# Performance work log

Measured on AMD Instinct MI355X. Metric: run time of the kernel, lower is better.

The kernel has to match this reference:

```python
import jax, jax.numpy as jnp
import numpy as np

D_MODEL = 1024
N_HEADS = 16
HEAD_DIM = D_MODEL // N_HEADS


def setup_inputs() -> dict:
    key = jax.random.key(0)
    k1, k2, k3 = jax.random.split(key, 3)
    B, T, C = 4, 2048, D_MODEL
    x = jax.random.normal(k1, (B, T, C), dtype=jnp.float32)
    # torch Linear weight is (out,in); store as (in,out) so y = x @ W
    w_qkv = jax.random.normal(k2, (C, 3 * C), dtype=jnp.float32) * (1.0 / np.sqrt(C))
    w_proj = jax.random.normal(k3, (C, C), dtype=jnp.float32) * (1.0 / np.sqrt(C))
    return {"x": x, "w_qkv": w_qkv, "w_proj": w_proj}


def reference(x, w_qkv, w_proj):
    B, T, C = x.shape
    H, Dh = N_HEADS, HEAD_DIM
    qkv = x @ w_qkv                        # (B,T,3C)
    q, k, v = jnp.split(qkv, 3, axis=-1)
    def heads(t):
        return t.reshape(B, T, H, Dh).transpose(0, 2, 1, 3)  # (B,H,T,Dh)
    q, k, v = heads(q), heads(k), heads(v)
    scores = jnp.einsum('bhqd,bhkd->bhqk', q, k) / np.sqrt(Dh).astype(np.float32)
    causal = jnp.tril(jnp.ones((T, T), dtype=bool))
    scores = jnp.where(causal, scores, -jnp.inf)
    attn = jax.nn.softmax(scores, axis=-1)
    y = jnp.einsum('bhqk,bhkd->bhqd', attn, v)  # (B,H,T,Dh)
    y = y.transpose(0, 2, 1, 3).reshape(B, T, C)
    return y @ w_proj
```

## Files before the change

kernel.cpp:

```cpp
#include <hip/hip_runtime.h>

#define SEQ_T 2048
#define NBATCH 4
#define CDIM 1024
#define NHEAD 16
#define MROWS 8192
#define QKVC 3072

typedef unsigned short u16;
typedef __bf16 bf16x8 __attribute__((ext_vector_type(8)));
typedef float f32x4 __attribute__((ext_vector_type(4)));
typedef float f32x16 __attribute__((ext_vector_type(16)));
typedef unsigned short u16x8 __attribute__((ext_vector_type(8)));
typedef unsigned uint32x4 __attribute__((ext_vector_type(4)));

__device__ __forceinline__ u16 f32_to_bf16(float f) {
  union { float f; unsigned int u; } v; v.f = f;
  unsigned int u = v.u;
  unsigned int r = ((u >> 16) & 1u) + 0x7fffu;
  return (u16)((u + r) >> 16);
}

__device__ __forceinline__ void gload_lds16(const u16* g, u16* l) {
  __builtin_amdgcn_global_load_lds(
      (const __attribute__((address_space(1))) void*)g,
      (__attribute__((address_space(3))) void*)l, 16, 0, 0);
}


__global__ __launch_bounds__(256) void cast_block_kernel(const float* __restrict__ in,
                                                         u16* __restrict__ out) {
  const int i = blockIdx.x * 256 + threadIdx.x;
  const int kg = i & 127;
  const int row = i >> 7;
  const float4 v0 = ((const float4*)in)[i * 2];
  const float4 v1 = ((const float4*)in)[i * 2 + 1];
  union { u16 u[8]; bf16x8 b; } o;
  o.u[0] = f32_to_bf16(v0.x); o.u[1] = f32_to_bf16(v0.y);
  o.u[2] = f32_to_bf16(v0.z); o.u[3] = f32_to_bf16(v0.w);
  o.u[4] = f32_to_bf16(v1.x); o.u[5] = f32_to_bf16(v1.y);
  o.u[6] = f32_to_bf16(v1.z); o.u[7] = f32_to_bf16(v1.w);
  const int tile = (row >> 4) * 32 + (kg >> 2);
  const int lane = (row & 15) + ((kg & 3) << 4);
  *(bf16x8*)(out + (size_t)tile * 512 + lane * 8) = o.b;
}

__global__ void transpose_cast_block_kernel(const float* __restrict__ in,
                                            u16* __restrict__ out, int Cc) {
  __shared__ float tile[32][33];
  const int c0 = blockIdx.x * 32, r0 = blockIdx.y * 32;
  const int tx = threadIdx.x, ty = threadIdx.y;
  #pragma unroll
  for (int i = 0; i < 32; i += 8)
    tile[ty + i][tx] = in[(size_t)(r0 + ty + i) * Cc + c0 + tx];
  __syncthreads();
  const int t = ty * 32 + tx;
  if (t < 128) {
    const int cc = t & 31, kgq = t >> 5;
    union { u16 u[8]; bf16x8 b; } o;
    #pragma unroll
    for (int j = 0; j < 8; ++j) o.u[j] = f32_to_bf16(tile[kgq * 8 + j][cc]);
    const int rowN = c0 + cc;
    const int tileI = (rowN >> 4) * 32 + (r0 >> 5);
    const int lane = (rowN & 15) + (kgq << 4);
    *(bf16x8*)(out + (size_t)tileI * 512 + lane * 8) = o.b;
  }
}

__global__ __launch_bounds__(256, 3)
void gemm1_kernel(const u16* __restrict__ Ab, const u16* __restrict__ Bb,
                  u16* __restrict__ Qb, u16* __restrict__ Kc, u16* __restrict__ Vc) {
  __shared__ u16 lds[24576];
  const int tid = threadIdx.x;
  const int lane = tid & 63, w = tid >> 6;
  const int wm = w >> 1, wn = w & 1;
  const int l15 = lane & 15, lhi = lane >> 4;
  const int row0 = blockIdx.x * 128, col0 = blockIdx.y * 128;
  const int rt0 = row0 >> 4, ct0 = col0 >> 4;

  const u16* aT = Ab + (size_t)(rt0 + w * 2) * 16384 + lane * 8;
  const u16* bT = Bb + (size_t)(ct0 + w * 2) * 16384 + lane * 8;

  f32x4 acc[4][4] = {};

#define SA(S) (lds + (S) * 4096)
#define SB(S) (lds + 12288 + (S) * 4096)
#define STAGE(KT, S)                                                            \
  {                                                                             \
    gload_lds16(aT + (size_t)(KT) * 512,         SA(S) + (w * 2) * 512);        \
    gload_lds16(aT + 16384 + (size_t)(KT) * 512, SA(S) + (w * 2 + 1) * 512);    \
    gload_lds16(bT + (size_t)(KT) * 512,         SB(S) + (w * 2) * 512);        \
    gload_lds16(bT + 16384 + (size_t)(KT) * 512, SB(S) + (w * 2 + 1) * 512);    \
  }
#define COMPUTE(S)                                                              \
  {                                                                             \
    bf16x8 af[4], bf[4];                                                        \
    _Pragma("unroll") for (int mi = 0; mi < 4; ++mi)                            \
      af[mi] = *(const bf16x8*)(SA(S) + (wm * 4 + mi) * 512 + lane * 8);        \
    _Pragma("unroll") for (int ni = 0; ni < 4; ++ni)                            \
      bf[ni] = *(const bf16x8*)(SB(S) + (wn * 4 + ni) * 512 + lane * 8);        \
    __builtin_amdgcn_s_setprio(1);                                              \
    _Pragma("unroll") for (int mi = 0; mi < 4; ++mi)                            \
      _Pragma("unroll") for (int ni = 0; ni < 4; ++ni)                          \
        acc[mi][ni] = __builtin_amdgcn_mfma_f32_16x16x32_bf16(af[mi], bf[ni],   \
                                                              acc[mi][ni], 0, 0, 0); \
    __builtin_amdgcn_s_setprio(0);                                              \
  }
#define WAITBAR4                                                                \
  asm volatile("s_waitcnt vmcnt(4)" ::: "memory");                              \
  __builtin_amdgcn_sched_barrier(0);                                            \
  __builtin_amdgcn_s_barrier();

  STAGE(0, 0);
  STAGE(1, 1);
  WAITBAR4;

  #pragma unroll 1
  for (int kt = 0; kt < 30; kt += 3) {
    STAGE(kt + 2, 2); COMPUTE(0); WAITBAR4;
    STAGE(kt + 3, 0); COMPUTE(1); WAITBAR4;
    STAGE(kt + 4, 1); COMPUTE(2); WAITBAR4;
  }
  COMPUTE(0);
  asm volatile("s_waitcnt vmcnt(0)" ::: "memory");
  __builtin_amdgcn_sched_barrier(0);
  __builtin_amdgcn_s_barrier();
  COMPUTE(1);
#undef STAGE
#undef COMPUTE
#undef WAITBAR4
#undef SA
#undef SB

  const int region = col0 >> 10;
  if (region == 0) {
    #pragma unroll
    for (int mt = 0; mt < 4; ++mt)
      #pragma unroll
      for (int nt = 0; nt < 4; ++nt)
        #pragma unroll
        for (int r = 0; r < 4; ++r) {
          const int rr = row0 + wm * 64 + mt * 16 + lhi * 4 + r;
          const int cc = col0 + wn * 64 + nt * 16 + l15;
          Qb[(size_t)rr * CDIM + cc] = f32_to_bf16(acc[mt][nt][r] * 0.18033688011f);
        }
  } else {
    __syncthreads();
    if (region == 1) {
      #pragma unroll
      for (int mt = 0; mt < 4; ++mt)
        #pragma unroll
        for (int nt = 0; nt < 4; ++nt)
          #pragma unroll
          for (int r = 0; r < 4; ++r) {
            const int sidx = wn * 8192 + (wm * 2 + (mt >> 1)) * 2048
                           + nt * 512
                           + ((mt & 1) * 16 + lhi * 4 + r + ((l15 >> 3) & 1) * 32) * 8
                           + (l15 & 7);
            lds[sidx] = f32_to_bf16(acc[mt][nt][r]);
          }
    } else {
      #pragma unroll
      for (int mt = 0; mt < 4; ++mt)
        #pragma unroll
        for (int nt = 0; nt < 4; ++nt)
          #pragma unroll
          for (int r = 0; r < 4; ++r) {
            const int sidx = wn * 8192 + (wm * 2 + (mt >> 1)) * 2048
                           + ((mt & 1) * 2 + (nt >> 1)) * 512
                           + ((nt & 1) * 16 + l15 + 32 * (lhi >> 1)) * 8
                           + (lhi & 1) * 4 + r;
            lds[sidx] = f32_to_bf16(acc[mt][nt][r]);
          }
    }
    __syncthreads();
    u16* dstB = (region == 1) ? Kc : Vc;
    const int bb = row0 >> 11;
    const int kv0b = (row0 & 2047) >> 5;
    const int hbase = (col0 & 1023) >> 6;
    #pragma unroll
    for (int hh = 0; hh < 2; ++hh) {
      u16* dst = dstB + (size_t)(bb * 16 + hbase + hh) * 131072 + (size_t)kv0b * 2048;
      const u16* src = lds + hh * 8192;
      #pragma unroll
      for (int c = 0; c < 4; ++c) {
        const int o = (c * 256 + tid) * 8;
        *(uint32x4*)(dst + o) = *(const uint32x4*)(src + o);
      }
    }
  }
}

__global__ __launch_bounds__(256, 3)
void gemm2_kernel(const u16* __restrict__ Ab, const u16* __restrict__ Bb,
                  float* __restrict__ C) {
  __shared__ u16 lds[24576];
  const int tid = threadIdx.x;
  const int lane = tid & 63, w = tid >> 6;
  const int wm = w >> 1, wn = w & 1;
  const int l15 = lane & 15, lhi = lane >> 4;
  const int row0 = blockIdx.x * 128, col0 = blockIdx.y * 128;
  const int rt0 = row0 >> 4, ct0 = col0 >> 4;

  const u16* aT = Ab + (size_t)(rt0 + w * 2) * 16384 + lane * 8;
  const u16* bT = Bb + (size_t)(ct0 + w * 2) * 16384 + lane * 8;

  f32x4 acc[4][4] = {};

#define SA(S) (lds + (S) * 4096)
#define SB(S) (lds + 12288 + (S) * 4096)
#define STAGE(KT, S)                                                            \
  {                                                                             \
    gload_lds16(aT + (size_t)(KT) * 512,         SA(S) + (w * 2) * 512);        \
    gload_lds16(aT + 16384 + (size_t)(KT) * 512, SA(S) + (w * 2 + 1) * 512);    \
    gload_lds16(bT + (size_t)(KT) * 512,         SB(S) + (w * 2) * 512);        \
    gload_lds16(bT + 16384 + (size_t)(KT) * 512, SB(S) + (w * 2 + 1) * 512);    \
  }
#define COMPUTE(S)                                                              \
  {                                                                             \
    bf16x8 af[4], bf[4];                                                        \
    _Pragma("unroll") for (int mi = 0; mi < 4; ++mi)                            \
      af[mi] = *(const bf16x8*)(SA(S) + (wm * 4 + mi) * 512 + lane * 8);        \
    _Pragma("unroll") for (int ni = 0; ni < 4; ++ni)                            \
      bf[ni] = *(const bf16x8*)(SB(S) + (wn * 4 + ni) * 512 + lane * 8);        \
    __builtin_amdgcn_s_setprio(1);                                              \
    _Pragma("unroll") for (int mi = 0; mi < 4; ++mi)                            \
      _Pragma("unroll") for (int ni = 0; ni < 4; ++ni)                          \
        acc[mi][ni] = __builtin_amdgcn_mfma_f32_16x16x32_bf16(af[mi], bf[ni],   \
                                                              acc[mi][ni], 0, 0, 0); \
    __builtin_amdgcn_s_setprio(0);                                              \
  }
#define WAITBAR4                                                                \
  asm volatile("s_waitcnt vmcnt(4)" ::: "memory");                              \
  __builtin_amdgcn_sched_barrier(0);                                            \
  __builtin_amdgcn_s_barrier();

  STAGE(0, 0);
  STAGE(1, 1);
  WAITBAR4;

  #pragma unroll 1
  for (int kt = 0; kt < 30; kt += 3) {
    STAGE(kt + 2, 2); COMPUTE(0); WAITBAR4;
    STAGE(kt + 3, 0); COMPUTE(1); WAITBAR4;
    STAGE(kt + 4, 1); COMPUTE(2); WAITBAR4;
  }
  COMPUTE(0);
  asm volatile("s_waitcnt vmcnt(0)" ::: "memory");
  __builtin_amdgcn_sched_barrier(0);
  __builtin_amdgcn_s_barrier();
  COMPUTE(1);
#undef STAGE
#undef COMPUTE
#undef WAITBAR4
#undef SA
#undef SB

  #pragma unroll
  for (int mt = 0; mt < 4; ++mt)
    #pragma unroll
    for (int nt = 0; nt < 4; ++nt)
      #pragma unroll
      for (int r = 0; r < 4; ++r) {
        const int rr = row0 + wm * 64 + mt * 16 + lhi * 4 + r;
        const int cc = col0 + wn * 64 + nt * 16 + l15;
        C[(size_t)rr * CDIM + cc] = acc[mt][nt][r];
      }
}

template <bool DOMASK>
__device__ __forceinline__ void attn_step32(const bf16x8 (&qf)[4],
                                            const bf16x8 (&kf)[4],
                                            const bf16x8 (&vb)[2][2],
                                            const bf16x8 ones,
                                            f32x16 (&acc)[2], f32x16& acc1,
                                            int l31, int lhi5, int kv0, int qg) {
  f32x16 st = {};
  #pragma unroll
  for (int i = 0; i < 4; ++i)
    st = __builtin_amdgcn_mfma_f32_32x32x16_bf16(kf[i], qf[i], st, 0, 0, 0);
  #pragma unroll
  for (int g = 0; g < 16; ++g) {
    float sv = st[g];
    if (DOMASK) {
      const int kvg = kv0 + (g & 3) + 8 * (g >> 2) + 4 * lhi5;
      sv = (kvg > qg) ? -__builtin_inff() : sv;
    }
    st[g] = exp2f(sv);
  }
  unsigned c0, c1, c2, c3, c4, c5, c6, c7;
  asm("v_cvt_pk_bf16_f32 %0, %1, %2" : "=v"(c0) : "v"(st[0]),  "v"(st[1]));
  asm("v_cvt_pk_bf16_f32 %0, %1, %2" : "=v"(c1) : "v"(st[2]),  "v"(st[3]));
  asm("v_cvt_pk_bf16_f32 %0, %1, %2" : "=v"(c2) : "v"(st[4]),  "v"(st[5]));
  asm("v_cvt_pk_bf16_f32 %0, %1, %2" : "=v"(c3) : "v"(st[6]),  "v"(st[7]));
  asm("v_cvt_pk_bf16_f32 %0, %1, %2" : "=v"(c4) : "v"(st[8]),  "v"(st[9]));
  asm("v_cvt_pk_bf16_f32 %0, %1, %2" : "=v"(c5) : "v"(st[10]), "v"(st[11]));
  asm("v_cvt_pk_bf16_f32 %0, %1, %2" : "=v"(c6) : "v"(st[12]), "v"(st[13]));
  asm("v_cvt_pk_bf16_f32 %0, %1, %2" : "=v"(c7) : "v"(st[14]), "v"(st[15]));
  asm("v_permlane32_swap_b32 %0, %1" : "+v"(c0), "+v"(c2));
  asm("v_permlane32_swap_b32 %0, %1" : "+v"(c1), "+v"(c3));
  asm("v_permlane32_swap_b32 %0, %1" : "+v"(c4), "+v"(c6));
  asm("v_permlane32_swap_b32 %0, %1" : "+v"(c5), "+v"(c7));
  uint32x4 p0w, p1w;
  p0w[0] = c0; p0w[1] = c1; p0w[2] = c2; p0w[3] = c3;
  p1w[0] = c4; p1w[1] = c5; p1w[2] = c6; p1w[3] = c7;
  const bf16x8 pa0 = __builtin_bit_cast(bf16x8, p0w);
  const bf16x8 pa1 = __builtin_bit_cast(bf16x8, p1w);
  acc[0] = __builtin_amdgcn_mfma_f32_32x32x16_bf16(pa0, vb[0][0], acc[0], 0, 0, 0);
  acc[0] = __builtin_amdgcn_mfma_f32_32x32x16_bf16(pa1, vb[1][0], acc[0], 0, 0, 0);
  acc[1] = __builtin_amdgcn_mfma_f32_32x32x16_bf16(pa0, vb[0][1], acc[1], 0, 0, 0);
  acc[1] = __builtin_amdgcn_mfma_f32_32x32x16_bf16(pa1, vb[1][1], acc[1], 0, 0, 0);
  acc1 = __builtin_amdgcn_mfma_f32_32x32x16_bf16(pa0, ones, acc1, 0, 0, 0);
  acc1 = __builtin_amdgcn_mfma_f32_32x32x16_bf16(pa1, ones, acc1, 0, 0, 0);
}

__global__ __launch_bounds__(256, 2) void attn_kernel(const u16* __restrict__ Qb,
                                                      const u16* __restrict__ Kc,
                                                      const u16* __restrict__ Vc,
                                                      u16* __restrict__ Yb) {
  __shared__ u16 Kl[2][4096];
  __shared__ u16 Vl[2][4096];
  const int tid = threadIdx.x, lane = tid & 63, wid = tid >> 6;
  const int l31 = lane & 31, lhi5 = lane >> 5;
  const int id = blockIdx.x;
  const int xcd = id & 7, graw = (id >> 3) & 7, hi3 = id >> 6;
  const int g = (hi3 & 4) ? (7 - graw) : graw;
  const int bh = hi3 * 8 + xcd;
  const int b = bh >> 4, h = bh & 15;
  const int pa = g * 4 + wid;
  const int qA0 = pa * 32, qB0 = (63 - pa) * 32;
  const int nchA = pa + 1, nchB = 64 - pa;
  const int nc2max = 32 - 2 * g;
  const u16* Qp  = Qb + (size_t)b * SEQ_T * CDIM + h * 64;
  const u16* KcC = Kc + (size_t)bh * 131072;
  const u16* VcC = Vc + (size_t)bh * 131072;

  u16x8 ou;
  #pragma unroll
  for (int j = 0; j < 8; ++j) ou[j] = 0x3F80;
  const bf16x8 ones = __builtin_bit_cast(bf16x8, ou);

  gload_lds16(KcC + wid * 512 + lane * 8,        &Kl[0][wid * 512]);
  gload_lds16(KcC + 2048 + wid * 512 + lane * 8, &Kl[0][2048 + wid * 512]);
  gload_lds16(VcC + wid * 512 + lane * 8,        &Vl[0][wid * 512]);
  gload_lds16(VcC + 2048 + wid * 512 + lane * 8, &Vl[0][2048 + wid * 512]);

  bf16x8 qfA[4], qfB[4];
  #pragma unroll
  for (int i = 0; i < 4; ++i) {
    qfA[i] = *(const bf16x8*)(Qp + (size_t)(qA0 + l31) * CDIM + i * 16 + lhi5 * 8);
    qfB[i] = *(const bf16x8*)(Qp + (size_t)(qB0 + l31) * CDIM + i * 16 + lhi5 * 8);
  }
  const int qgA = qA0 + l31, qgB = qB0 + l31;

  f32x16 accA[2] = {}, accB[2] = {};
  f32x16 acc1A = {}, acc1B = {};

  __syncthreads();

  int cbuf = 0;
  for (int ic2 = 0; ic2 < nc2max; ++ic2) {
    if (ic2 + 1 < nc2max) {
      const u16* kg = KcC + (size_t)(ic2 + 1) * 4096 + wid * 512 + lane * 8;
      const u16* vg = VcC + (size_t)(ic2 + 1) * 4096 + wid * 512 + lane * 8;
      gload_lds16(kg,        &Kl[cbuf ^ 1][wid * 512]);
      gload_lds16(kg + 2048, &Kl[cbuf ^ 1][2048 + wid * 512]);
      gload_lds16(vg,        &Vl[cbuf ^ 1][wid * 512]);
      gload_lds16(vg + 2048, &Vl[cbuf ^ 1][2048 + wid * 512]);
    }
    #pragma unroll
    for (int h2 = 0; h2 < 2; ++h2) {
      const int c = ic2 * 2 + h2;
      const u16* kb = &Kl[cbuf][h2 * 2048];
      const u16* vp = &Vl[cbuf][h2 * 2048];
      bf16x8 kf[4], vb[2][2];
      #pragma unroll
      for (int i = 0; i < 4; ++i)
        kf[i] = *(const bf16x8*)(kb + i * 512 + lane * 8);
      #pragma unroll
      for (int kk = 0; kk < 2; ++kk)
        #pragma unroll
        for (int dh = 0; dh < 2; ++dh)
          vb[kk][dh] = *(const bf16x8*)(vp + (kk * 2 + dh) * 512 + lane * 8);

      const int kv0 = c * 32;
      if (c < nchB) {
        if (c == nchB - 1)
          attn_step32<true>(qfB, kf, vb, ones, accB, acc1B, l31, lhi5, kv0, qgB);
        else
          attn_step32<false>(qfB, kf, vb, ones, accB, acc1B, l31, lhi5, kv0, qgB);
      }
      if (c < nchA) {
        if (c == nchA - 1)
          attn_step32<true>(qfA, kf, vb, ones, accA, acc1A, l31, lhi5, kv0, qgA);
        else
          attn_step32<false>(qfA, kf, vb, ones, accA, acc1A, l31, lhi5, kv0, qgA);
      }
    }
    __syncthreads();
    cbuf ^= 1;
  }

  #pragma unroll
  for (int g2 = 0; g2 < 16; ++g2) {
    const int qlA = (g2 & 3) + 8 * (g2 >> 2) + 4 * lhi5;
    const float ivA = 1.0f / acc1A[g2];
    const float ivB = 1.0f / acc1B[g2];
    const int laneb = ((qlA & 15)) + ((l31 >> 3) << 4);
    const int jj = l31 & 7;
    #pragma unroll
    for (int dh = 0; dh < 2; ++dh) {
      const int qA = qA0 + qlA;
      const int qB = qB0 + qlA;
      const size_t rrA = (size_t)b * 2048 + qA;
      const size_t rrB = (size_t)b * 2048 + qB;
      Yb[((rrA >> 4) * 32 + h * 2 + dh) * 512 + laneb * 8 + jj] =
          f32_to_bf16(accA[dh][g2] * ivA);
      Yb[((rrB >> 4) * 32 + h * 2 + dh) * 512 + laneb * 8 + jj] =
          f32_to_bf16(accB[dh][g2] * ivB);
    }
  }
}

extern "C" void kernel_launch(void* const* d_in, const int* in_sizes, int n_in,
                              void* d_out, int out_size, void* d_ws, size_t ws_size,
                              hipStream_t stream) {
  const float* x      = (const float*)d_in[0];
  const float* w_qkv  = (const float*)d_in[1];
  const float* w_proj = (const float*)d_in[2];
  float* out = (float*)d_out;

  u16* Xb  = (u16*)d_ws;
  u16* Wqt = Xb  + (size_t)MROWS * CDIM;
  u16* Wpt = Wqt + (size_t)QKVC * CDIM;
  u16* Qb  = Wpt + (size_t)CDIM * CDIM;
  u16* Kc  = Qb  + (size_t)MROWS * CDIM;
  u16* Vc  = Kc  + (size_t)64 * 131072;
  u16* Yb  = Vc  + (size_t)64 * 131072;

  cast_block_kernel<<<MROWS * CDIM / 8 / 256, 256, 0, stream>>>(x, Xb);
  transpose_cast_block_kernel<<<dim3(QKVC / 32, CDIM / 32), dim3(32, 8), 0, stream>>>(w_qkv, Wqt, QKVC);
  transpose_cast_block_kernel<<<dim3(CDIM / 32, CDIM / 32), dim3(32, 8), 0, stream>>>(w_proj, Wpt, CDIM);

  gemm1_kernel<<<dim3(MROWS / 128, QKVC / 128), 256, 0, stream>>>(Xb, Wqt, Qb, Kc, Vc);

  attn_kernel<<<512, 256, 0, stream>>>(Qb, Kc, Vc, Yb);

  gemm2_kernel<<<dim3(MROWS / 128, CDIM / 128), 256, 0, stream>>>(Yb, Wpt, out);
}
```

Baseline: 158.9 us.

## Give each attention wave one query tile and double the grid

The attention kernel now assigns each wave a single 32-row query tile, where before each wave handled a pair of causally balanced tiles. Blocks combine two low and two high tiles so total work stays balanced, and the grid doubles to 1024 blocks with launch bounds raised to 4 blocks per CU. This cuts register pressure to raise occupancy and spreads work over more blocks. In exchange, K/V tiles are loaded into LDS twice as often in total, the K/V fragments read from LDS are shared by one query tile instead of two, and waves in a block finish at different times and idle at the barriers.

```diff
diff --git a/kernel.cpp b/kernel.cpp
--- a/kernel.cpp
+++ b/kernel.cpp
@@ -314,7 +314,7 @@
   acc1 = __builtin_amdgcn_mfma_f32_32x32x16_bf16(pa1, ones, acc1, 0, 0, 0);
 }
 
-__global__ __launch_bounds__(256, 2) void attn_kernel(const u16* __restrict__ Qb,
+__global__ __launch_bounds__(256, 4) void attn_kernel(const u16* __restrict__ Qb,
                                                       const u16* __restrict__ Kc,
                                                       const u16* __restrict__ Vc,
                                                       u16* __restrict__ Yb) {
@@ -323,14 +323,14 @@
   const int tid = threadIdx.x, lane = tid & 63, wid = tid >> 6;
   const int l31 = lane & 31, lhi5 = lane >> 5;
   const int id = blockIdx.x;
-  const int xcd = id & 7, graw = (id >> 3) & 7, hi3 = id >> 6;
-  const int g = (hi3 & 4) ? (7 - graw) : graw;
+  const int xcd = id & 7, g = (id >> 3) & 15, hi3 = id >> 7;
   const int bh = hi3 * 8 + xcd;
   const int b = bh >> 4, h = bh & 15;
-  const int pa = g * 4 + wid;
-  const int qA0 = pa * 32, qB0 = (63 - pa) * 32;
-  const int nchA = pa + 1, nchB = 64 - pa;
-  const int nc2max = 32 - 2 * g;
+  const int jw = (wid == 0) ? 2 * g : (wid == 1) ? 2 * g + 1
+               : (wid == 2) ? 63 - 2 * g : 62 - 2 * g;
+  const int q0 = jw * 32;
+  const int nch = jw + 1;
+  const int nc2max = 32 - g;
   const u16* Qp  = Qb + (size_t)b * SEQ_T * CDIM + h * 64;
   const u16* KcC = Kc + (size_t)bh * 131072;
   const u16* VcC = Vc + (size_t)bh * 131072;
@@ -345,16 +345,14 @@
   gload_lds16(VcC + wid * 512 + lane * 8,        &Vl[0][wid * 512]);
   gload_lds16(VcC + 2048 + wid * 512 + lane * 8, &Vl[0][2048 + wid * 512]);
 
-  bf16x8 qfA[4], qfB[4];
-  #pragma unroll
-  for (int i = 0; i < 4; ++i) {
-    qfA[i] = *(const bf16x8*)(Qp + (size_t)(qA0 + l31) * CDIM + i * 16 + lhi5 * 8);
-    qfB[i] = *(const bf16x8*)(Qp + (size_t)(qB0 + l31) * CDIM + i * 16 + lhi5 * 8);
-  }
-  const int qgA = qA0 + l31, qgB = qB0 + l31;
-
-  f32x16 accA[2] = {}, accB[2] = {};
-  f32x16 acc1A = {}, acc1B = {};
+  bf16x8 qf[4];
+  #pragma unroll
+  for (int i = 0; i < 4; ++i)
+    qf[i] = *(const bf16x8*)(Qp + (size_t)(q0 + l31) * CDIM + i * 16 + lhi5 * 8);
+  const int qg = q0 + l31;
+
+  f32x16 acc[2] = {};
+  f32x16 acc1 = {};
 
   __syncthreads();
 
@@ -371,30 +369,24 @@
     #pragma unroll
     for (int h2 = 0; h2 < 2; ++h2) {
       const int c = ic2 * 2 + h2;
-      const u16* kb = &Kl[cbuf][h2 * 2048];
-      const u16* vp = &Vl[cbuf][h2 * 2048];
-      bf16x8 kf[4], vb[2][2];
-      #pragma unroll
-      for (int i = 0; i < 4; ++i)
-        kf[i] = *(const bf16x8*)(kb + i * 512 + lane * 8);
-      #pragma unroll
-      for (int kk = 0; kk < 2; ++kk)
+      if (c < nch) {
+        const u16* kb = &Kl[cbuf][h2 * 2048];
+        const u16* vp = &Vl[cbuf][h2 * 2048];
+        bf16x8 kf[4], vb[2][2];
         #pragma unroll
-        for (int dh = 0; dh < 2; ++dh)
-          vb[kk][dh] = *(const bf16x8*)(vp + (kk * 2 + dh) * 512 + lane * 8);
-
-      const int kv0 = c * 32;
-      if (c < nchB) {
-        if (c == nchB - 1)
-          attn_step32<true>(qfB, kf, vb, ones, accB, acc1B, l31, lhi5, kv0, qgB);
+        for (int i = 0; i < 4; ++i)
+          kf[i] = *(const bf16x8*)(kb + i * 512 + lane * 8);
+        #pragma unroll
+        for (int kk = 0; kk < 2; ++kk)
+          #pragma unroll
+          for (int dh = 0; dh < 2; ++dh)
+            vb[kk][dh] = *(const bf16x8*)(vp + (kk * 2 + dh) * 512 + lane * 8);
+
+        const int kv0 = c * 32;
+        if (c == nch - 1)
+          attn_step32<true>(qf, kf, vb, ones, acc, acc1, l31, lhi5, kv0, qg);
         else
-          attn_step32<false>(qfB, kf, vb, ones, accB, acc1B, l31, lhi5, kv0, qgB);
-      }
-      if (c < nchA) {
-        if (c == nchA - 1)
-          attn_step32<true>(qfA, kf, vb, ones, accA, acc1A, l31, lhi5, kv0, qgA);
-        else
-          attn_step32<false>(qfA, kf, vb, ones, accA, acc1A, l31, lhi5, kv0, qgA);
+          attn_step32<false>(qf, kf, vb, ones, acc, acc1, l31, lhi5, kv0, qg);
       }
     }
     __syncthreads();
@@ -403,22 +395,15 @@
 
   #pragma unroll
   for (int g2 = 0; g2 < 16; ++g2) {
-    const int qlA = (g2 & 3) + 8 * (g2 >> 2) + 4 * lhi5;
-    const float ivA = 1.0f / acc1A[g2];
-    const float ivB = 1.0f / acc1B[g2];
-    const int laneb = ((qlA & 15)) + ((l31 >> 3) << 4);
+    const int ql = (g2 & 3) + 8 * (g2 >> 2) + 4 * lhi5;
+    const float iv = 1.0f / acc1[g2];
+    const int laneb = (ql & 15) + ((l31 >> 3) << 4);
     const int jj = l31 & 7;
-    #pragma unroll
-    for (int dh = 0; dh < 2; ++dh) {
-      const int qA = qA0 + qlA;
-      const int qB = qB0 + qlA;
-      const size_t rrA = (size_t)b * 2048 + qA;
-      const size_t rrB = (size_t)b * 2048 + qB;
-      Yb[((rrA >> 4) * 32 + h * 2 + dh) * 512 + laneb * 8 + jj] =
-          f32_to_bf16(accA[dh][g2] * ivA);
-      Yb[((rrB >> 4) * 32 + h * 2 + dh) * 512 + laneb * 8 + jj] =
-          f32_to_bf16(accB[dh][g2] * ivB);
-    }
+    const size_t rr = (size_t)b * 2048 + q0 + ql;
+    #pragma unroll
+    for (int dh = 0; dh < 2; ++dh)
+      Yb[((rr >> 4) * 32 + h * 2 + dh) * 512 + laneb * 8 + jj] =
+          f32_to_bf16(acc[dh][g2] * iv);
   }
 }
 
@@ -444,7 +429,7 @@
 
   gemm1_kernel<<<dim3(MROWS / 128, QKVC / 128), 256, 0, stream>>>(Xb, Wqt, Qb, Kc, Vc);
 
-  attn_kernel<<<512, 256, 0, stream>>>(Qb, Kc, Vc, Yb);
+  attn_kernel<<<1024, 256, 0, stream>>>(Qb, Kc, Vc, Yb);
 
   gemm2_kernel<<<dim3(MROWS / 128, CDIM / 128), 256, 0, stream>>>(Yb, Wpt, out);
 }
```

After: 163.0 us. +2.6%, slower.
